# Kernel optimization log

Measured on AMD Instinct MI355X. Metric: run time of the kernel, lower is better.

## Reference

```python
import jax, jax.numpy as jnp
import numpy as np
import math

BS, SL, NE, NH = 4, 2048, 1024, 16
HD = NE // NH  # 64


def setup_inputs() -> dict:
    key = jax.random.key(0)
    ks = jax.random.split(key, 5)
    x = jax.random.normal(ks[0], (BS, SL, NE), dtype=jnp.float32)
    # causal mask: 1 where attending allowed (j <= i), 0 otherwise
    mask = jnp.tril(jnp.ones((SL, SL), dtype=jnp.int32))[None, None, :, :]
    s = 1.0 / math.sqrt(NE)
    Wqkv = jax.random.normal(ks[1], (NE, 3 * NE), dtype=jnp.float32) * s
    bqkv = jax.random.normal(ks[2], (3 * NE,), dtype=jnp.float32) * 0.02
    Wo = jax.random.normal(ks[3], (NE, NE), dtype=jnp.float32) * s
    bo = jax.random.normal(ks[4], (NE,), dtype=jnp.float32) * 0.02
    return {"x": x, "mask": mask, "Wqkv": Wqkv, "bqkv": bqkv, "Wo": Wo, "bo": bo}


def reference(x, mask, Wqkv, bqkv, Wo, bo):
    bs, sl, ne = x.shape
    qkv = x @ Wqkv + bqkv                       # [bs, sl, 3*ne]
    q, k, v = jnp.split(qkv, 3, axis=-1)
    # [bs, sl, ne] -> [bs, nh, sl, hd]
    q = q.reshape(bs, sl, NH, HD).transpose(0, 2, 1, 3)
    k = k.reshape(bs, sl, NH, HD).transpose(0, 2, 1, 3)
    v = v.reshape(bs, sl, NH, HD).transpose(0, 2, 1, 3)
    scale = 1.0 / math.sqrt(HD)
    att = jnp.einsum('bhqd,bhkd->bhqk', q, k) * scale  # [bs, nh, sl, sl]
    att = jnp.where(mask == 0, -jnp.inf, att)
    w = jax.nn.softmax(att, axis=-1)
    y = jnp.einsum('bhqk,bhkd->bhqd', w, v)            # [bs, nh, sl, hd]
    y = y.transpose(0, 2, 1, 3).reshape(bs, sl, ne)
    return y @ Wo + bo
```

## Files before the change

kernel.cpp:

```cpp
#include <hip/hip_runtime.h>

#define BS 4
#define SL 2048
#define NE 1024
#define NH 16
#define HD 64
#define N3 3072

typedef __attribute__((ext_vector_type(8))) __bf16 bf16x8;
typedef __attribute__((ext_vector_type(4))) float f32x4;
typedef __attribute__((ext_vector_type(4))) short s16x4;
typedef unsigned short u16;

__device__ __forceinline__ u16 f2bf(float f) {
  union { float f; unsigned int u; } v; v.f = f;
  unsigned int r = v.u + 0x7FFFu + ((v.u >> 16) & 1u);
  return (u16)(r >> 16);
}
__device__ __forceinline__ int pack_bf2(float a, float b) {
  union { float f; unsigned int u; } x, y; x.f = a; y.f = b;
  return (int)((y.u & 0xFFFF0000u) | (x.u >> 16));
}

__device__ __forceinline__ void gld16(const void* g, void* l) {
#if __has_builtin(__builtin_amdgcn_global_load_lds)
  __builtin_amdgcn_global_load_lds(
      (const __attribute__((address_space(1))) unsigned int*)g,
      (__attribute__((address_space(3))) unsigned int*)l, 16, 0, 0);
#else
  *(int4*)((char*)l + (size_t)(threadIdx.x & 63) * 16) = *(const int4*)g;
#endif
}

__global__ void convert_x(const float* __restrict__ x, u16* __restrict__ xb) {
  int i = (blockIdx.x * 256 + threadIdx.x) * 8;
  float4 f0 = *(const float4*)(x + i);
  float4 f1 = *(const float4*)(x + i + 4);
  union { int4 v; u16 h[8]; } p;
  p.h[0] = f2bf(f0.x); p.h[1] = f2bf(f0.y);
  p.h[2] = f2bf(f0.z); p.h[3] = f2bf(f0.w);
  p.h[4] = f2bf(f1.x); p.h[5] = f2bf(f1.y);
  p.h[6] = f2bf(f1.z); p.h[7] = f2bf(f1.w);
  *(int4*)(xb + i) = p.v;
}

__global__ void transpose_w(const float* __restrict__ W, u16* __restrict__ Wt,
                            int K, int N) {
  __shared__ u16 tile[32][33];
  int bn = blockIdx.x * 32, bk = blockIdx.y * 32;
  int tx = threadIdx.x, ty = threadIdx.y;
  for (int r = 0; r < 32; r += 8)
    tile[ty + r][tx] = f2bf(W[(size_t)(bk + ty + r) * N + bn + tx]);
  __syncthreads();
  for (int r = 0; r < 32; r += 8)
    Wt[(size_t)(bn + ty + r) * K + bk + tx] = tile[tx][ty + r];
}

#define VMW(n) asm volatile("s_waitcnt vmcnt(" #n ")" ::: "memory")
#define BARR()                         \
  do {                                 \
    __builtin_amdgcn_s_barrier();      \
    __builtin_amdgcn_sched_barrier(0); \
  } while (0)
#define MFMA_G(a, b, c) \
  __builtin_amdgcn_mfma_f32_16x16x32_bf16(a, b, c, 0, 0, 0)

template <int C32, int BN>
__global__ __launch_bounds__(512, 2) void gemm8p(
    const u16* __restrict__ A, const u16* __restrict__ Bt,
    const float* __restrict__ bias, void* __restrict__ C, int M, int N, int K,
    int lda) {
  constexpr int BM = 256, BK = 64;
  constexpr int NF = BN / 64;
  constexpr int NHALF = NF / 2;
  __shared__ u16 As[2][BM * BK];
  __shared__ u16 Bs[2][BN * BK];

  const int tid = threadIdx.x;
  const int w = tid >> 6, lane = tid & 63;
  const int lq = lane >> 4, lr = lane & 15;
  const int m0 = blockIdx.y * BM, n0 = blockIdx.x * BN;

  const int l8 = lane >> 3, lb = lane & 7;
  const int swz8 = ((lb ^ l8) * 8);
  const u16* gA = A + (size_t)(m0 + w * 16 + l8) * lda + swz8;
  const u16* gB =
      (BN == 256) ? Bt + (size_t)(n0 + w * 16 + l8) * K + swz8
                  : Bt + (size_t)(n0 + w * 8 + l8) * K + swz8;

#define STAGE_A(buf, half, gp)                                        \
  do {                                                                \
    gld16((gp) + (size_t)((half) * 128) * lda,                        \
          &As[buf][(half) * 8192 + (2 * w) * 512]);                   \
    gld16((gp) + (size_t)((half) * 128 + 8) * lda,                    \
          &As[buf][(half) * 8192 + (2 * w + 1) * 512]);               \
  } while (0)
#define STAGE_B(buf, half, gp)                                        \
  do {                                                                \
    if constexpr (BN == 256) {                                        \
      gld16((gp) + (size_t)((half) * 128) * K,                        \
            &Bs[buf][(half) * 8192 + (2 * w) * 512]);                 \
      gld16((gp) + (size_t)((half) * 128 + 8) * K,                    \
            &Bs[buf][(half) * 8192 + (2 * w + 1) * 512]);             \
    } else {                                                          \
      gld16((gp) + (size_t)((half) * 64) * K,                         \
            &Bs[buf][(half) * 4096 + w * 512]);                       \
    }                                                                 \
  } while (0)
#define READ_A(buf, half)                                                    \
  _Pragma("unroll") for (int i = 0; i < 4; i++) _Pragma("unroll") for (       \
      int ks = 0; ks < 2; ks++) {                                            \
    int row = (half) * 128 + (w >> 2) * 64 + i * 16 + lr;                    \
    a[i][ks] =                                                               \
        *(const bf16x8*)&As[buf][row * 64 + (((ks * 4 + lq) ^ (lr & 7)) * 8)]; \
  }
#define READ_B(buf, nh)                                                      \
  _Pragma("unroll") for (int jj = 0; jj < NHALF; jj++) _Pragma("unroll") for ( \
      int ks = 0; ks < 2; ks++) {                                            \
    int row = (BN == 256) ? ((nh) * 128 + (w & 3) * 32 + jj * 16 + lr)       \
                          : ((nh) * 64 + (w & 3) * 16 + lr);                 \
    bb[nh][jj][ks] =                                                         \
        *(const bf16x8*)&Bs[buf][row * 64 + (((ks * 4 + lq) ^ (lr & 7)) * 8)]; \
  }
#define MFMA_PHASE(ilo, nh)                                                  \
  do {                                                                       \
    __builtin_amdgcn_s_setprio(1);                                          \
    _Pragma("unroll") for (int i = 0; i < 4; i++) _Pragma("unroll") for (     \
        int jj = 0; jj < NHALF; jj++) _Pragma("unroll") for (int ks = 0;     \
                                                             ks < 2; ks++)   \
        acc[(ilo) + i][(nh)*NHALF + jj] = MFMA_G(                            \
            a[i][ks], bb[nh][jj][ks], acc[(ilo) + i][(nh)*NHALF + jj]);      \
    __builtin_amdgcn_s_setprio(0);                                          \
  } while (0)

  const f32x4 fzero = {0.f, 0.f, 0.f, 0.f};
  f32x4 acc[8][NF];
#pragma unroll
  for (int i = 0; i < 8; i++)
#pragma unroll
    for (int j = 0; j < NF; j++) acc[i][j] = fzero;

  const int KT = K / BK;
  STAGE_A(0, 0, gA);
  STAGE_B(0, 0, gB);
  STAGE_B(0, 1, gB);
  STAGE_A(0, 1, gA);
  const u16* gAn = gA + BK;
  const u16* gBn = gB + BK;

  for (int T = 0; T < KT; T++) {
    const int cur = T & 1, nxt = cur ^ 1;
    const bool pf = (T + 1 < KT);
    bf16x8 a[4][2], bb[2][NHALF][2];
    if (BN == 256) { VMW(4); } else { VMW(3); }
    BARR();
    READ_A(cur, 0);
    READ_B(cur, 0);
    if (pf) STAGE_A(nxt, 0, gAn);
    MFMA_PHASE(0, 0);
    if (pf) { VMW(4); } else { VMW(2); }
    BARR();
    READ_B(cur, 1);
    if (pf) STAGE_B(nxt, 0, gBn);
    MFMA_PHASE(0, 1);
    if (pf) {
      if (BN == 256) { VMW(4); } else { VMW(3); }
    } else {
      VMW(0);
    }
    BARR();
    READ_A(cur, 1);
    if (pf) STAGE_B(nxt, 1, gBn);
    MFMA_PHASE(4, 1);
    if (pf) STAGE_A(nxt, 1, gAn);
    MFMA_PHASE(4, 0);
    gAn += BK;
    gBn += BK;
  }

#pragma unroll
  for (int j = 0; j < NF; j++) {
    int col;
    if (BN == 256)
      col = n0 + (j >> 1) * 128 + (w & 3) * 32 + (j & 1) * 16 + lr;
    else
      col = n0 + j * 64 + (w & 3) * 16 + lr;
    float bv = bias[col];
#pragma unroll
    for (int i = 0; i < 8; i++) {
      int rbase = m0 + (i >> 2) * 128 + (w >> 2) * 64 + (i & 3) * 16 + lq * 4;
#pragma unroll
      for (int r = 0; r < 4; r++) {
        float val = acc[i][j][r] + bv;
        if (C32) ((float*)C)[(size_t)(rbase + r) * N + col] = val;
        else     ((u16*)C)[(size_t)(rbase + r) * N + col]   = f2bf(val);
      }
    }
  }
#undef STAGE_A
#undef STAGE_B
#undef READ_A
#undef READ_B
#undef MFMA_PHASE
}

#define KSTR 72
#define MFMA16(a, b, c) __builtin_amdgcn_mfma_f32_16x16x32_bf16(a, b, c, 0, 0, 0)
#define MFMA1616(a, b, c) \
  __builtin_amdgcn_mfma_f32_16x16x16bf16_1k(a, b, c, 0, 0, 0)

__device__ __forceinline__ void attn_step(const bf16x8& q0, const bf16x8& q1,
                                          const u16* __restrict__ Kb,
                                          const u16* __restrict__ Vs,
                                          bool diag, int w, int lq, int lr,
                                          f32x4 (&o)[4], float& m_, float& l_) {
  const f32x4 fzero = {0.f, 0.f, 0.f, 0.f};
  const int swz = (lq ^ (lr & 3)) * 8;
  f32x4 s[4];
  __builtin_amdgcn_s_setprio(1);
#pragma unroll
  for (int j = 0; j < 4; j++) {
    int kr = j * 16 + lr;
    bf16x8 kf0 = *(const bf16x8*)&Kb[kr * 32 + swz];
    bf16x8 kf1 = *(const bf16x8*)&Kb[2048 + kr * 32 + swz];
    f32x4 z = MFMA16(kf0, q0, fzero);
    s[j] = MFMA16(kf1, q1, z);
  }
  __builtin_amdgcn_s_setprio(0);
  if (diag) {
    int qloc = w * 16 + lr - 4 * lq;
#pragma unroll
    for (int j = 0; j < 4; j++)
#pragma unroll
      for (int r = 0; r < 4; r++)
        if (16 * j + r > qloc) s[j][r] = -1e30f;
  }
  float mt = s[0][0];
#pragma unroll
  for (int j = 0; j < 4; j++)
#pragma unroll
    for (int r = 0; r < 4; r++) mt = fmaxf(mt, s[j][r]);
  mt = fmaxf(mt, __shfl_xor(mt, 16));
  mt = fmaxf(mt, __shfl_xor(mt, 32));
  float mn = m_;
  if (!__all(mt <= m_ + 64.0f)) {
    mn = fmaxf(m_, mt);
    float alpha = __expf((m_ - mn) * 0.125f);
    m_ = mn;
    l_ *= alpha;
#pragma unroll
    for (int jd = 0; jd < 4; jd++)
#pragma unroll
      for (int r = 0; r < 4; r++) o[jd][r] *= alpha;
  }
  s16x4 pa[4];
  float psum = 0.f;
#pragma unroll
  for (int j = 0; j < 4; j++) {
    float p0 = __expf((s[j][0] - mn) * 0.125f);
    float p1 = __expf((s[j][1] - mn) * 0.125f);
    float p2 = __expf((s[j][2] - mn) * 0.125f);
    float p3 = __expf((s[j][3] - mn) * 0.125f);
    psum += (p0 + p1) + (p2 + p3);
    union { int i[2]; s16x4 v; } pu;
    pu.i[0] = pack_bf2(p0, p1);
    pu.i[1] = pack_bf2(p2, p3);
    pa[j] = pu.v;
  }
  l_ += psum;
  __builtin_amdgcn_s_setprio(1);
#pragma unroll
  for (int jd = 0; jd < 4; jd++) {
    const u16* vrow = &Vs[(jd * 16 + lr) * KSTR + lq * 16];
    union { int4 q; s16x4 h[2]; } va, vb;
    va.q = *(const int4*)vrow;
    vb.q = *(const int4*)(vrow + 8);
    o[jd] = MFMA1616(va.h[0], pa[0], o[jd]);
    o[jd] = MFMA1616(va.h[1], pa[1], o[jd]);
    o[jd] = MFMA1616(vb.h[0], pa[2], o[jd]);
    o[jd] = MFMA1616(vb.h[1], pa[3], o[jd]);
  }
  __builtin_amdgcn_s_setprio(0);
}

__global__ __launch_bounds__(256, 4) void attn_paired(u16* __restrict__ qkv) {
  __shared__ u16 Ks[2][4096];
  __shared__ u16 Vs[64 * KSTR];

  const int tid = threadIdx.x;
  const int w = tid >> 6, lane = tid & 63;
  const int lq = lane >> 4, lr = lane & 15;
  const int bh = blockIdx.x, p = blockIdx.y;
  const int h = bh & (NH - 1), b = bh >> 4;
  const int qt0 = p, qt1 = (SL / 64 - 1) - p;

  u16* base = qkv + (size_t)b * SL * N3;
  const u16* kbase = base + NE + h * HD;

  const int kg_key = lane >> 2;
  const int kg_blk = (lane & 3) ^ (kg_key & 3);
  const int skey = tid & 63, sd0 = (tid >> 6) * 8;
  const int skeyP = ((skey >> 2) & 3) * 16 + (skey >> 4) * 4 + (skey & 3);
  const u16* vrow0 = base + (size_t)skey * N3 + 2 * NE + h * HD + sd0;

#define KPRE(buf, key0)                                                     \
  {                                                                         \
    _Pragma("unroll") for (int t = 0; t < 2; t++) {                         \
      int chunk = w * 2 + t, half = chunk >> 2, kgrp = chunk & 3;           \
      const u16* g = kbase + (size_t)((key0) + kgrp * 16 + kg_key) * N3 +   \
                     half * 32 + kg_blk * 8;                                \
      gld16(g, &Ks[buf][half * 2048 + kgrp * 512]);                         \
    }                                                                       \
  }

  bf16x8 qf[2][2];
#pragma unroll
  for (int half = 0; half < 2; half++) {
    int qt = half ? qt1 : qt0;
    const u16* qrow = base + (size_t)(qt * 64 + w * 16 + lr) * N3 + h * HD;
    qf[half][0] = *(const bf16x8*)(qrow + lq * 8);
    qf[half][1] = *(const bf16x8*)(qrow + 32 + lq * 8);
  }

  const f32x4 fzero = {0.f, 0.f, 0.f, 0.f};
  f32x4 o[2][4];
  float m_[2], l_[2];
#pragma unroll
  for (int half = 0; half < 2; half++) {
    m_[half] = -1e30f;
    l_[half] = 0.f;
#pragma unroll
    for (int jd = 0; jd < 4; jd++) o[half][jd] = fzero;
  }

  KPRE(0, 0);
  int4 v0 = *(const int4*)vrow0;
  int4 v1 = *(const int4*)(vrow0 + 32);

  const int ktend = qt1 + 1;
  for (int kt = 0; kt < ktend; kt++) {
    __syncthreads();
    {
      union { int4 v; u16 u[8]; } t0, t1;
      t0.v = v0; t1.v = v1;
#pragma unroll
      for (int j = 0; j < 8; j++) {
        Vs[(sd0 + j) * KSTR + skeyP] = t0.u[j];
        Vs[(sd0 + 32 + j) * KSTR + skeyP] = t1.u[j];
      }
    }
    __syncthreads();

    if (kt + 1 < ktend) {
      KPRE((kt + 1) & 1, (kt + 1) * 64);
      const u16* nv = vrow0 + (size_t)(kt + 1) * 64 * N3;
      v0 = *(const int4*)nv;
      v1 = *(const int4*)(nv + 32);
    }

    const u16* Kb = &Ks[kt & 1][0];
    attn_step(qf[1][0], qf[1][1], Kb, Vs, kt == qt1, w, lq, lr, o[1], m_[1],
              l_[1]);
    if (kt <= qt0)
      attn_step(qf[0][0], qf[0][1], Kb, Vs, kt == qt0, w, lq, lr, o[0], m_[0],
                l_[0]);
  }

#pragma unroll
  for (int half = 0; half < 2; half++) {
    int qt = half ? qt1 : qt0;
    float lsum = l_[half];
    lsum += __shfl_xor(lsum, 16);
    lsum += __shfl_xor(lsum, 32);
    float inv = 1.0f / lsum;
    u16* yrow = base + (size_t)(qt * 64 + w * 16 + lr) * N3 + h * HD;
#pragma unroll
    for (int jd = 0; jd < 4; jd++) {
      int2 val;
      val.x = (int)(((unsigned)f2bf(o[half][jd][1] * inv) << 16) |
                    f2bf(o[half][jd][0] * inv));
      val.y = (int)(((unsigned)f2bf(o[half][jd][3] * inv) << 16) |
                    f2bf(o[half][jd][2] * inv));
      *(int2*)(yrow + 16 * jd + 4 * lq) = val;
    }
  }
}

extern "C" void kernel_launch(void* const* d_in, const int* in_sizes, int n_in,
                              void* d_out, int out_size, void* d_ws,
                              size_t ws_size, hipStream_t stream) {
  const float* x    = (const float*)d_in[0];
  const float* Wqkv = (const float*)d_in[2];
  const float* bqkv = (const float*)d_in[3];
  const float* Wo   = (const float*)d_in[4];
  const float* bo   = (const float*)d_in[5];

  u16* WqkvT  = (u16*)d_ws;
  u16* WoT    = WqkvT + (size_t)N3 * NE;
  u16* xb     = WoT + (size_t)NE * NE;
  u16* qkvbuf = xb + (size_t)BS * SL * NE;

  convert_x<<<(BS * SL * NE) / (256 * 8), 256, 0, stream>>>(x, xb);
  transpose_w<<<dim3(N3 / 32, NE / 32), dim3(32, 8), 0, stream>>>(Wqkv, WqkvT,
                                                                  NE, N3);
  transpose_w<<<dim3(NE / 32, NE / 32), dim3(32, 8), 0, stream>>>(Wo, WoT, NE,
                                                                  NE);
  gemm8p<0, 256><<<dim3(N3 / 256, (BS * SL) / 256), 512, 0, stream>>>(
      xb, WqkvT, bqkv, qkvbuf, BS * SL, N3, NE, NE);
  attn_paired<<<dim3(BS * NH, SL / 128), 256, 0, stream>>>(qkvbuf);
  gemm8p<1, 128><<<dim3(NE / 128, (BS * SL) / 256), 512, 0, stream>>>(
      qkvbuf, WoT, bo, d_out, BS * SL, NE, NE, N3);
}
```

Measured before the change: 268.9 us.

## Restructure GEMM K-loop barriers into mid/end phases with LDS waits

Reworks the synchronization schedule of the double-buffered bf16 GEMM K-loop. It adds barriers after each LDS read batch, drains lgkmcnt before the MFMA phases, and moves the vmcnt waits to the end of each phase, including a prologue wait and a trailing wait at the loop bottom. The goal is to line up the waves so the LDS reads and the global-to-LDS prefetches interleave more evenly with the MFMA phases. The cost is roughly twice as many workgroup barriers per iteration, which can add stalls.

```diff
diff --git a/kernel.cpp b/kernel.cpp
--- a/kernel.cpp
+++ b/kernel.cpp
@@ -30,6 +30,18 @@
 #else
   *(int4*)((char*)l + (size_t)(threadIdx.x & 63) * 16) = *(const int4*)g;
 #endif
+}
+
+template <int N>
+__device__ __forceinline__ void vmw() {
+  if constexpr (N == 0)
+    asm volatile("s_waitcnt vmcnt(0)" ::: "memory");
+  else if constexpr (N == 2)
+    asm volatile("s_waitcnt vmcnt(2)" ::: "memory");
+  else if constexpr (N == 3)
+    asm volatile("s_waitcnt vmcnt(3)" ::: "memory");
+  else if constexpr (N == 4)
+    asm volatile("s_waitcnt vmcnt(4)" ::: "memory");
 }
 
 __global__ void convert_x(const float* __restrict__ x, u16* __restrict__ xb) {
@@ -56,11 +68,16 @@
     Wt[(size_t)(bn + ty + r) * K + bk + tx] = tile[tx][ty + r];
 }
 
-#define VMW(n) asm volatile("s_waitcnt vmcnt(" #n ")" ::: "memory")
-#define BARR()                         \
-  do {                                 \
-    __builtin_amdgcn_s_barrier();      \
-    __builtin_amdgcn_sched_barrier(0); \
+#define BARR_MID()                                      \
+  do {                                                  \
+    __builtin_amdgcn_s_barrier();                       \
+    asm volatile("s_waitcnt lgkmcnt(0)" ::: "memory");  \
+    __builtin_amdgcn_sched_barrier(0);                  \
+  } while (0)
+#define BARR_END()                                      \
+  do {                                                  \
+    __builtin_amdgcn_s_barrier();                       \
+    __builtin_amdgcn_sched_barrier(0);                  \
   } while (0)
 #define MFMA_G(a, b, c) \
   __builtin_amdgcn_mfma_f32_16x16x32_bf16(a, b, c, 0, 0, 0)
@@ -73,6 +90,9 @@
   constexpr int BM = 256, BK = 64;
   constexpr int NF = BN / 64;
   constexpr int NHALF = NF / 2;
+  constexpr int V0 = (BN == 256) ? 4 : 3;
+  constexpr int V1 = 4;
+  constexpr int V2 = (BN == 256) ? 4 : 3;
   __shared__ u16 As[2][BM * BK];
   __shared__ u16 Bs[2][BN * BK];
 
@@ -147,33 +167,36 @@
   STAGE_A(0, 1, gA);
   const u16* gAn = gA + BK;
   const u16* gBn = gB + BK;
+  vmw<V0>();
+  BARR_END();
 
   for (int T = 0; T < KT; T++) {
     const int cur = T & 1, nxt = cur ^ 1;
     const bool pf = (T + 1 < KT);
     bf16x8 a[4][2], bb[2][NHALF][2];
-    if (BN == 256) { VMW(4); } else { VMW(3); }
-    BARR();
     READ_A(cur, 0);
     READ_B(cur, 0);
     if (pf) STAGE_A(nxt, 0, gAn);
+    BARR_MID();
     MFMA_PHASE(0, 0);
-    if (pf) { VMW(4); } else { VMW(2); }
-    BARR();
+    if (pf) vmw<V1>(); else vmw<2>();
+    BARR_END();
     READ_B(cur, 1);
     if (pf) STAGE_B(nxt, 0, gBn);
+    BARR_MID();
     MFMA_PHASE(0, 1);
-    if (pf) {
-      if (BN == 256) { VMW(4); } else { VMW(3); }
-    } else {
-      VMW(0);
-    }
-    BARR();
+    if (pf) vmw<V2>(); else vmw<0>();
+    BARR_END();
     READ_A(cur, 1);
     if (pf) STAGE_B(nxt, 1, gBn);
+    BARR_MID();
     MFMA_PHASE(4, 1);
+    BARR_END();
     if (pf) STAGE_A(nxt, 1, gAn);
+    BARR_MID();
     MFMA_PHASE(4, 0);
+    if (pf) vmw<V0>();
+    BARR_END();
     gAn += BK;
     gBn += BK;
   }
```

Result: slower. 275.8 us (+2.6%).
